# Kernel tuning notes

Hardware: AMD Instinct MI355X
Metric: run time of the kernel (lower is better)

The kernel has to match this reference:

```python
import jax, jax.numpy as jnp
import numpy as np

OUT_SIZE = 7
SPATIAL_SCALE = 0.0625
SAMPLE_NUM = 2


def setup_inputs() -> dict:
    key = jax.random.key(0)
    k1, k2, k3, k4, k5, k6 = jax.random.split(key, 6)
    N, C, H, W = 4, 256, 96, 96
    K = 1024
    features = jax.random.normal(k1, (N, C, H, W), dtype=jnp.float32)
    img_h, img_w = H / SPATIAL_SCALE, W / SPATIAL_SCALE
    batch_idx = jax.random.randint(k2, (K,), 0, N).astype(jnp.float32)
    x1 = jax.random.uniform(k3, (K,)) * (img_w - 320.0)
    y1 = jax.random.uniform(k4, (K,)) * (img_h - 320.0)
    x2 = x1 + 16.0 + jax.random.uniform(k5, (K,)) * 300.0
    y2 = y1 + 16.0 + jax.random.uniform(k6, (K,)) * 300.0
    rois = jnp.stack([batch_idx, x1, y1, x2, y2], axis=1).astype(jnp.float32)
    return {"features": features, "rois": rois}


def _sample_coords(start, bin_size):
    # start, bin_size: [K]; returns [K, OUT_SIZE*SAMPLE_NUM] sample-point coords
    g = jnp.arange(OUT_SIZE * SAMPLE_NUM, dtype=jnp.float32)
    bin_idx = jnp.floor(g / SAMPLE_NUM)
    sub = g - bin_idx * SAMPLE_NUM
    offs = bin_idx + (sub + 0.5) / SAMPLE_NUM
    return start[:, None] + bin_size[:, None] * offs[None, :]


def _interp_1d(coord, size):
    # coord: [K, G] sample coords along one axis of a map of length `size`.
    valid = (coord >= -1.0) & (coord <= jnp.float32(size))
    c = jnp.clip(coord, 0.0, jnp.float32(size - 1))
    lo = jnp.floor(c)
    hi = jnp.minimum(lo + 1.0, jnp.float32(size - 1))
    frac = c - lo  # weight of hi; (1-frac) weight of lo
    return lo.astype(jnp.int32), hi.astype(jnp.int32), frac, valid


def roi_align(features, rois):
    N, C, H, W = features.shape
    b = rois[:, 0].astype(jnp.int32)
    x1, y1, x2, y2 = (rois[:, i] * SPATIAL_SCALE for i in (1, 2, 3, 4))
    roi_w = jnp.maximum(x2 - x1, 1.0)
    roi_h = jnp.maximum(y2 - y1, 1.0)
    bin_w = roi_w / OUT_SIZE
    bin_h = roi_h / OUT_SIZE

    ys = _sample_coords(y1, bin_h)  # [K, G]
    xs = _sample_coords(x1, bin_w)  # [K, G]
    ylo, yhi, fy, vy = _interp_1d(ys, H)
    xlo, xhi, fx, vx = _interp_1d(xs, W)

    bb = b[:, None, None]

    def gather(yi, xi):
        # -> [K, G, G, C]
        return features[bb, :, yi[:, :, None], xi[:, None, :]]

    wy_lo, wy_hi = (1.0 - fy), fy
    wx_lo, wx_hi = (1.0 - fx), fx

    def w2(wy, wx):
        return (wy[:, :, None] * wx[:, None, :])[..., None]

    val = (gather(ylo, xlo) * w2(wy_lo, wx_lo)
           + gather(ylo, xhi) * w2(wy_lo, wx_hi)
           + gather(yhi, xlo) * w2(wy_hi, wx_lo)
           + gather(yhi, xhi) * w2(wy_hi, wx_hi))
    mask = (vy[:, :, None] & vx[:, None, :])[..., None]
    val = jnp.where(mask, val, 0.0)

    K = rois.shape[0]
    G = OUT_SIZE * SAMPLE_NUM
    val = val.reshape(K, OUT_SIZE, SAMPLE_NUM, OUT_SIZE, SAMPLE_NUM, C)
    out = val.mean(axis=(2, 4))          # average the sample points per bin
    return jnp.transpose(out, (0, 3, 1, 2))  # [K, C, out, out]


def reference(features, rois):
    return roi_align(features, rois)
```

## Files before the change

### kernel.cpp

```cpp
#include <hip/hip_runtime.h>

#define CCH   256
#define FH    96
#define FW    96
#define SCALE 0.0625f

#define HWIN  23
#define PC    24
#define CHW   (HWIN*PC)
#define CC    8
#define NCHUNK (CCH/CC)

__global__ __launch_bounds__(256, 4)
void roialign_kernel(const float* __restrict__ feat,
                     const float* __restrict__ rois,
                     float* __restrict__ out)
{
    __shared__ __align__(16) float win[CC * CHW];
    __shared__ int   s_lo[2][14];
    __shared__ float s_wl[2][14], s_wh[2][14];

    const int k   = blockIdx.x;
    const int tid = threadIdx.x;

    const float x1 = rois[k*5+1] * SCALE;
    const float y1 = rois[k*5+2] * SCALE;
    const float x2 = rois[k*5+3] * SCALE;
    const float y2 = rois[k*5+4] * SCALE;
    const int   b  = (int)rois[k*5+0];
    const float binw = fmaxf(x2 - x1, 1.0f) * (1.0f/7.0f);
    const float binh = fmaxf(y2 - y1, 1.0f) * (1.0f/7.0f);

    if (tid < 28) {
        const int   axis  = (tid >= 14) ? 1 : 0;
        const int   g     = axis ? tid - 14 : tid;
        const float start = axis ? x1 : y1;
        const float bsz   = axis ? binw : binh;
        const float offs  = (float)(g >> 1) + 0.25f + 0.5f*(float)(g & 1);
        const float coord = start + bsz * offs;
        const bool  valid = (coord >= -1.0f) && (coord <= 96.0f);
        const float cc    = fminf(fmaxf(coord, 0.0f), 95.0f);
        const float lof   = floorf(cc);
        const float frac  = cc - lof;
        const float v     = valid ? 1.0f : 0.0f;
        s_lo[axis][g] = (int)lof;
        s_wl[axis][g] = (1.0f - frac) * v;
        s_wh[axis][g] = frac * v;
    }
    __syncthreads();

    const int row0 = s_lo[0][0];
    const int col0 = s_lo[1][0] & ~3;
    const int hwin = min(s_lo[0][13] + 1, 95) - row0 + 1;

    for (int i = tid; i < CC*PC; i += 256) {
        const int cl  = i / PC;
        const int col = i - cl*PC;
        win[cl*CHW + hwin*PC + col] = 0.0f;
    }

    const int  pix    = tid & 63;
    const int  cg     = tid >> 6;
    const bool active = pix < 49;
    const int  p      = active ? pix : 0;
    const int  oy     = p / 7;
    const int  ox     = p - oy*7;

    int   addr0[4];
    float w00[4], w01[4], w10[4], w11[4];
    #pragma unroll
    for (int sy = 0; sy < 2; ++sy) {
        const int   gy  = 2*oy + sy;
        const int   rlo = s_lo[0][gy] - row0;
        const float wyl = s_wl[0][gy], wyh = s_wh[0][gy];
        #pragma unroll
        for (int sx = 0; sx < 2; ++sx) {
            const int   gx  = 2*ox + sx;
            const int   clo = s_lo[1][gx] - col0;
            const float wxl = s_wl[1][gx], wxh = s_wh[1][gx];
            const int   s   = sy*2 + sx;
            addr0[s] = cg*CHW + rlo*PC + clo;
            w00[s] = wyl*wxl;  w01[s] = wyl*wxh;
            w10[s] = wyh*wxl;  w11[s] = wyh*wxh;
        }
    }

    const int  lcl     = tid >> 5;
    const int  ll      = tid & 31;
    const int  lr0     = ll / 6;
    const int  lq      = ll - lr0*6;
    const bool lactive = ll < 30;
    const int  colg    = min(col0 + lq*4, FW - 4);

    float* outp = out + ((size_t)k*CCH + cg)*49 + p;

    for (int ch = 0; ch < NCHUNK; ++ch) {
        const int cbase = ch*CC;
        if (lactive) {
            const float* gp = feat + (((b*CCH + cbase + lcl)*FH + row0 + lr0)*FW + colg);
            float*       wp = &win[lcl*CHW + lr0*PC + lq*4];
            for (int r = lr0; r < hwin; r += 5) {
                *(float4*)wp = *(const float4*)gp;
                gp += 5*FW;
                wp += 5*PC;
            }
        }
        __syncthreads();

        if (active) {
            float acc0 = 0.0f, acc1 = 0.0f;
            #pragma unroll
            for (int s = 0; s < 4; ++s) {
                const int a  = addr0[s];
                const int a2 = a + 4*CHW;
                acc0 += w00[s]*win[a]      + w01[s]*win[a+1]
                      + w10[s]*win[a+PC]   + w11[s]*win[a+PC+1];
                acc1 += w00[s]*win[a2]     + w01[s]*win[a2+1]
                      + w10[s]*win[a2+PC]  + w11[s]*win[a2+PC+1];
            }
            outp[0]    = acc0 * 0.25f;
            outp[4*49] = acc1 * 0.25f;
        }
        __syncthreads();
        outp += CC*49;
    }
}

extern "C" void kernel_launch(void* const* d_in, const int* in_sizes, int n_in,
                              void* d_out, int out_size, void* d_ws, size_t ws_size,
                              hipStream_t stream) {
    const float* feat = (const float*)d_in[0];
    const float* rois = (const float*)d_in[1];
    float*       outp = (float*)d_out;
    const int K = in_sizes[1] / 5;
    roialign_kernel<<<K, 256, 0, stream>>>(feat, rois, outp);
}
```

Measured before the change: 160.0 us.

## Split channels across two blocks per ROI and prefetch next chunk into registers

Each ROI is now handled by two blocks, each covering half the channels, which doubles the grid and raises the occupancy hint to 8 blocks per CU. Global loads for the next channel chunk are issued into register staging before the interpolation compute on the current chunk, and are written to shared memory after the barrier. This overlaps global memory latency with compute and drops one barrier per iteration. In exchange it uses more registers and always performs five float4 loads per thread, with rows beyond the window clamped and redirected to a padding row.

```diff
diff --git a/kernel.cpp b/kernel.cpp
--- a/kernel.cpp
+++ b/kernel.cpp
@@ -9,9 +9,10 @@
 #define PC    24
 #define CHW   (HWIN*PC)
 #define CC    8
-#define NCHUNK (CCH/CC)
+#define HALFCH 128
+#define NCHUNK (HALFCH/CC)
 
-__global__ __launch_bounds__(256, 4)
+__global__ __launch_bounds__(256, 8)
 void roialign_kernel(const float* __restrict__ feat,
                      const float* __restrict__ rois,
                      float* __restrict__ out)
@@ -20,8 +21,9 @@
     __shared__ int   s_lo[2][14];
     __shared__ float s_wl[2][14], s_wh[2][14];
 
-    const int k   = blockIdx.x;
-    const int tid = threadIdx.x;
+    const int k    = blockIdx.x >> 1;
+    const int half = blockIdx.x & 1;
+    const int tid  = threadIdx.x;
 
     const float x1 = rois[k*5+1] * SCALE;
     const float y1 = rois[k*5+2] * SCALE;
@@ -87,25 +89,44 @@
 
     const int  lcl     = tid >> 5;
     const int  ll      = tid & 31;
-    const int  lr0     = ll / 6;
-    const int  lq      = ll - lr0*6;
+    const int  lr0     = min(ll / 6, 4);
+    const int  lq      = ll - (ll/6)*6;
     const bool lactive = ll < 30;
     const int  colg    = min(col0 + lq*4, FW - 4);
+    const int  cbase0  = half * HALFCH;
 
-    float* outp = out + ((size_t)k*CCH + cg)*49 + p;
+    const float* gbase = feat + ((size_t)(b*CCH + cbase0 + lcl)*FH)*FW + colg;
+
+    float4 stage[5];
+    int    grow[5];
+    int    ldst[5];
+    #pragma unroll
+    for (int i = 0; i < 5; ++i) {
+        const int r = lr0 + 5*i;
+        grow[i] = min(row0 + r, FH - 1) * FW;
+        ldst[i] = lcl*CHW + ((r < hwin) ? r : 22)*PC + lq*4;
+    }
+
+    #define ISSUE_LOADS(CH)  do {                                           \
+        const float* gp = gbase + (size_t)(CH)*CC*FH*FW;                    \
+        _Pragma("unroll")                                                   \
+        for (int i = 0; i < 5; ++i) stage[i] = *(const float4*)(gp + grow[i]); \
+    } while (0)
+
+    float* outp = out + ((size_t)k*CCH + cbase0 + cg)*49 + p;
+
+    if (lactive) ISSUE_LOADS(0);
 
     for (int ch = 0; ch < NCHUNK; ++ch) {
-        const int cbase = ch*CC;
+        if (ch) __syncthreads();
         if (lactive) {
-            const float* gp = feat + (((b*CCH + cbase + lcl)*FH + row0 + lr0)*FW + colg);
-            float*       wp = &win[lcl*CHW + lr0*PC + lq*4];
-            for (int r = lr0; r < hwin; r += 5) {
-                *(float4*)wp = *(const float4*)gp;
-                gp += 5*FW;
-                wp += 5*PC;
-            }
+            #pragma unroll
+            for (int i = 0; i < 5; ++i)
+                *(float4*)&win[ldst[i]] = stage[i];
         }
         __syncthreads();
+
+        if (ch + 1 < NCHUNK && lactive) ISSUE_LOADS(ch + 1);
 
         if (active) {
             float acc0 = 0.0f, acc1 = 0.0f;
@@ -121,9 +142,9 @@
             outp[0]    = acc0 * 0.25f;
             outp[4*49] = acc1 * 0.25f;
         }
-        __syncthreads();
         outp += CC*49;
     }
+    #undef ISSUE_LOADS
 }
 
 extern "C" void kernel_launch(void* const* d_in, const int* in_sizes, int n_in,
@@ -133,5 +154,5 @@
     const float* rois = (const float*)d_in[1];
     float*       outp = (float*)d_out;
     const int K = in_sizes[1] / 5;
-    roialign_kernel<<<K, 256, 0, stream>>>(feat, rois, outp);
+    roialign_kernel<<<K*2, 256, 0, stream>>>(feat, rois, outp);
 }
```

New measurement: 413.3 us. 158% more time.

## Give each wave a private LDS window, prefetch channels in registers, split ROI across blocks

Applied to the files above, without the earlier changes.

Each ROI is now handled by two blocks of 128 channels each. Every wave owns a private shared-memory plane and walks 32 channels on its own, so the block-wide __syncthreads between load and compute disappear. The next channel's window is prefetched into registers while the current one is interpolated, and the 1/4 averaging is folded into the weights. Correctness relies on wave-synchronous LDS ordering and on the clamped 21x24 window always covering the ROI footprint. Occupancy is raised to 8 blocks per SM.

```diff
diff --git a/kernel.cpp b/kernel.cpp
--- a/kernel.cpp
+++ b/kernel.cpp
@@ -3,25 +3,28 @@
 #define CCH   256
 #define FH    96
 #define FW    96
+#define HW    (FH*FW)
 #define SCALE 0.0625f
 
-#define HWIN  23
-#define PC    24
-#define CHW   (HWIN*PC)
-#define CC    8
-#define NCHUNK (CCH/CC)
+#define HROWS 21
+#define PSTR  28
+#define PLANE (HROWS*PSTR)
+#define WCH   32
 
-__global__ __launch_bounds__(256, 4)
+__global__ __launch_bounds__(256, 8)
 void roialign_kernel(const float* __restrict__ feat,
                      const float* __restrict__ rois,
                      float* __restrict__ out)
 {
-    __shared__ __align__(16) float win[CC * CHW];
+    __shared__ __align__(16) float win[4 * PLANE];
     __shared__ int   s_lo[2][14];
     __shared__ float s_wl[2][14], s_wh[2][14];
 
-    const int k   = blockIdx.x;
-    const int tid = threadIdx.x;
+    const int k    = blockIdx.x >> 1;
+    const int half = blockIdx.x & 1;
+    const int tid  = threadIdx.x;
+    const int w    = tid >> 6;
+    const int ll   = tid & 63;
 
     const float x1 = rois[k*5+1] * SCALE;
     const float y1 = rois[k*5+2] * SCALE;
@@ -50,79 +53,86 @@
     __syncthreads();
 
     const int row0 = s_lo[0][0];
-    const int col0 = s_lo[1][0] & ~3;
-    const int hwin = min(s_lo[0][13] + 1, 95) - row0 + 1;
+    const int col0 = min(s_lo[1][0] & ~3, FW - 24);
+    int hw_        = min(s_lo[0][13] + 1, FH-1) - row0 + 1;
+    const int hwin = min(hw_, HROWS);
+    const int nslot = hwin * 6;
 
-    for (int i = tid; i < CC*PC; i += 256) {
-        const int cl  = i / PC;
-        const int col = i - cl*PC;
-        win[cl*CHW + hwin*PC + col] = 0.0f;
+    float* const wp = &win[w * PLANE];
+
+    {
+        const float4 z = make_float4(0.f, 0.f, 0.f, 0.f);
+        #pragma unroll
+        for (int j = 0; j < 3; ++j) {
+            const int q = ll + 64*j;
+            if (q < PLANE/4) *(float4*)&wp[q*4] = z;
+        }
     }
 
-    const int  pix    = tid & 63;
-    const int  cg     = tid >> 6;
-    const bool active = pix < 49;
-    const int  p      = active ? pix : 0;
-    const int  oy     = p / 7;
-    const int  ox     = p - oy*7;
+    const bool active = ll < 49;
+    const int  p  = active ? ll : 0;
+    const int  oy = p / 7;
+    const int  ox = p - oy*7;
 
-    int   addr0[4];
+    int   aL[4], aH[4];
     float w00[4], w01[4], w10[4], w11[4];
     #pragma unroll
     for (int sy = 0; sy < 2; ++sy) {
         const int   gy  = 2*oy + sy;
-        const int   rlo = s_lo[0][gy] - row0;
+        const int   rlo = min(s_lo[0][gy] - row0,                 HROWS-1);
+        const int   rhi = min(min(s_lo[0][gy]+1, FH-1) - row0,    HROWS-1);
         const float wyl = s_wl[0][gy], wyh = s_wh[0][gy];
         #pragma unroll
         for (int sx = 0; sx < 2; ++sx) {
             const int   gx  = 2*ox + sx;
-            const int   clo = s_lo[1][gx] - col0;
+            const int   clo = min(s_lo[1][gx] - col0, PSTR-2);
             const float wxl = s_wl[1][gx], wxh = s_wh[1][gx];
             const int   s   = sy*2 + sx;
-            addr0[s] = cg*CHW + rlo*PC + clo;
-            w00[s] = wyl*wxl;  w01[s] = wyl*wxh;
-            w10[s] = wyh*wxl;  w11[s] = wyh*wxh;
+            aL[s] = rlo*PSTR + clo;
+            aH[s] = rhi*PSTR + clo;
+            w00[s] = wyl*wxl*0.25f;  w01[s] = wyl*wxh*0.25f;
+            w10[s] = wyh*wxl*0.25f;  w11[s] = wyh*wxh*0.25f;
         }
     }
 
-    const int  lcl     = tid >> 5;
-    const int  ll      = tid & 31;
-    const int  lr0     = ll / 6;
-    const int  lq      = ll - lr0*6;
-    const bool lactive = ll < 30;
-    const int  colg    = min(col0 + lq*4, FW - 4);
+    const int  sl1 = ll + 64;
+    const int  r0  = ll  / 6, q0 = ll  - r0*6;
+    const int  r1  = sl1 / 6, q1 = sl1 - r1*6;
+    const bool L0  = ll  < nslot;
+    const bool L1  = sl1 < nslot;
+    const int  goff0 = min(row0 + r0, FH-1)*FW + col0 + q0*4;
+    const int  goff1 = min(row0 + r1, FH-1)*FW + col0 + q1*4;
+    const int  ld0   = min(r0, HROWS-1)*PSTR + q0*4;
+    const int  ld1   = min(r1, HROWS-1)*PSTR + q1*4;
 
-    float* outp = out + ((size_t)k*CCH + cg)*49 + p;
+    const int    cb   = half*128 + w*WCH;
+    const float* gch  = feat + (size_t)(b*CCH + cb) * HW;
+    float*       outp = out  + ((size_t)k*CCH + cb)*49 + p;
 
-    for (int ch = 0; ch < NCHUNK; ++ch) {
-        const int cbase = ch*CC;
-        if (lactive) {
-            const float* gp = feat + (((b*CCH + cbase + lcl)*FH + row0 + lr0)*FW + colg);
-            float*       wp = &win[lcl*CHW + lr0*PC + lq*4];
-            for (int r = lr0; r < hwin; r += 5) {
-                *(float4*)wp = *(const float4*)gp;
-                gp += 5*FW;
-                wp += 5*PC;
-            }
+    float4 st0, st1;
+    if (L0) st0 = *(const float4*)(gch + goff0);
+    if (L1) st1 = *(const float4*)(gch + goff1);
+
+    for (int c = 0; c < WCH; ++c) {
+        if (L0) *(float4*)&wp[ld0] = st0;
+        if (L1) *(float4*)&wp[ld1] = st1;
+
+        if (c + 1 < WCH) {
+            const float* gn = gch + (size_t)(c+1)*HW;
+            if (L0) st0 = *(const float4*)(gn + goff0);
+            if (L1) st1 = *(const float4*)(gn + goff1);
         }
-        __syncthreads();
 
         if (active) {
-            float acc0 = 0.0f, acc1 = 0.0f;
+            float acc = 0.0f;
             #pragma unroll
             for (int s = 0; s < 4; ++s) {
-                const int a  = addr0[s];
-                const int a2 = a + 4*CHW;
-                acc0 += w00[s]*win[a]      + w01[s]*win[a+1]
-                      + w10[s]*win[a+PC]   + w11[s]*win[a+PC+1];
-                acc1 += w00[s]*win[a2]     + w01[s]*win[a2+1]
-                      + w10[s]*win[a2+PC]  + w11[s]*win[a2+PC+1];
+                acc += w00[s]*wp[aL[s]]   + w01[s]*wp[aL[s]+1]
+                     + w10[s]*wp[aH[s]]   + w11[s]*wp[aH[s]+1];
             }
-            outp[0]    = acc0 * 0.25f;
-            outp[4*49] = acc1 * 0.25f;
+            outp[0] = acc;
         }
-        __syncthreads();
-        outp += CC*49;
+        outp += 49;
     }
 }
 
@@ -133,5 +143,5 @@
     const float* rois = (const float*)d_in[1];
     float*       outp = (float*)d_out;
     const int K = in_sizes[1] / 5;
-    roialign_kernel<<<K, 256, 0, stream>>>(feat, rois, outp);
+    roialign_kernel<<<K*2, 256, 0, stream>>>(feat, rois, outp);
 }
```

New measurement: 135.6 us. 1.18x faster.
